# Optimization experiments

Measured on AMD Instinct MI355X. Metric: run time of the kernel, lower is better.

The kernel has to match this reference:

```python
import jax, jax.numpy as jnp
import numpy as np
from math import log

B, L, D = 2, 4096, 2048
H, Dh, C, KW = 16, 128, 64, 4
EPS = 1e-5
SCALE = 0.02


def setup_inputs() -> dict:
    key = jax.random.key(0)
    ks = jax.random.split(key, 16)
    rn = lambda k, shp, sc=SCALE: jax.random.normal(k, shp, jnp.float32) * sc
    # dt_bias built like the torch module
    dt = jnp.exp(jax.random.uniform(ks[7], (H,)) * (log(0.1) - log(0.001)) + log(0.001))
    dt = jnp.clip(dt, 0.0001, None)
    dt_bias = dt + jnp.log(-jnp.expm1(-dt))
    return {
        "x": jax.random.normal(ks[0], (B, L, D), jnp.float32),
        "Wq": rn(ks[1], (H * Dh, D)),
        "Wk": rn(ks[2], (H * Dh, D)),
        "Wv": rn(ks[3], (H * Dh, D)),
        "Wb": rn(ks[4], (H, D)),
        "Wa": rn(ks[5], (H, D)),
        "A_log": jnp.log(jax.random.uniform(ks[6], (H,), minval=0.01, maxval=16.0)),
        "dt_bias": dt_bias,
        "conv_q": rn(ks[8], (H * Dh, 1, KW), 0.2),
        "conv_k": rn(ks[9], (H * Dh, 1, KW), 0.2),
        "conv_v": rn(ks[10], (H * Dh, 1, KW), 0.2),
        "Wg": rn(ks[11], (H * Dh, D)),
        "norm_w": jnp.ones((Dh,), jnp.float32),
        "Wo": rn(ks[12], (D, H * Dh)),
        "S0": jnp.zeros((B, H, Dh, Dh), jnp.float32),
    }


def _causal_dwconv(x, w):
    # x: [B,L,Ch]; w: [Ch,1,KW] depthwise causal conv (left pad KW-1), then SiLU
    y = jax.lax.conv_general_dilated(
        x.transpose(0, 2, 1), w, (1,), [(KW - 1, 0)],
        feature_group_count=w.shape[0], dimension_numbers=("NCH", "OIH", "NCH"))
    return jax.nn.silu(y).transpose(0, 2, 1)


def reference(x, Wq, Wk, Wv, Wb, Wa, A_log, dt_bias, conv_q, conv_k, conv_v, Wg, norm_w, Wo, S0):
    q = _causal_dwconv(x @ Wq.T, conv_q).reshape(B, L, H, Dh).transpose(0, 2, 1, 3)  # [B,H,L,Dh]
    k = _causal_dwconv(x @ Wk.T, conv_k).reshape(B, L, H, Dh).transpose(0, 2, 1, 3)
    v = _causal_dwconv(x @ Wv.T, conv_v).reshape(B, L, H, Dh).transpose(0, 2, 1, 3)
    beta = jax.nn.sigmoid(x @ Wb.T).transpose(0, 2, 1)                                # [B,H,L]
    g = (-jnp.exp(A_log) * jax.nn.softplus(x @ Wa.T + dt_bias)).transpose(0, 2, 1)    # [B,H,L]
    l2 = lambda t: t / jnp.maximum(jnp.linalg.norm(t, axis=-1, keepdims=True), 1e-12)
    q = l2(q) / (Dh ** 0.5)
    k = l2(k)

    N = L // C  # chunks (L divisible by C)
    chop = lambda t: jnp.moveaxis(t.reshape(B, H, N, C, Dh), 2, 0)   # [N,B,H,C,Dh]
    qc, kc, vc = chop(q), chop(k), chop(v)
    betac = jnp.moveaxis(beta.reshape(B, H, N, C), 2, 0)[..., None]  # [N,B,H,C,1]
    gc = jnp.moveaxis(g.reshape(B, H, N, C), 2, 0)                   # [N,B,H,C]

    eye = jnp.eye(C, dtype=x.dtype)
    m_incl = jnp.tril(jnp.ones((C, C), bool))
    m_strict = jnp.tril(jnp.ones((C, C), bool), -1)

    def step(S, ch):
        Q, Kc, V, bet, gch = ch
        lg = jnp.cumsum(gch, axis=-1)          # log gamma, [B,H,C]
        gamma = jnp.exp(lg)
        lgC = lg[..., -1:]
        gCr = jnp.exp(lgC - lg)
        gammaC = jnp.exp(lgC)[..., None]       # [B,H,1,1]
        Qd = Q * gamma[..., None]
        Kd = gCr[..., None] * Kc
        Sd = S * gammaC
        Gam = lg[..., :, None] - lg[..., None, :]
        ratio = jnp.exp(jnp.where(m_strict, Gam, -jnp.inf))
        A = eye + bet * ratio * (Kc @ jnp.swapaxes(Kc, -1, -2))
        T = jax.scipy.linalg.solve_triangular(A, jnp.broadcast_to(eye, A.shape), lower=True)
        Wm = T @ (bet * gamma[..., None] * Kc)
        U = T @ (bet * V)
        St = jnp.swapaxes(S, -1, -2)
        GM = jnp.exp(jnp.where(m_incl, Gam, -jnp.inf))
        mid = U - Wm @ St                      # [B,H,C,Dh]
        O = Qd @ St + ((Q @ jnp.swapaxes(Kc, -1, -2)) * GM) @ mid
        S_new = Sd + jnp.swapaxes(mid, -1, -2) @ Kd
        return S_new, O

    S_fin, Os = jax.lax.scan(step, S0, (qc, kc, vc, betac, gc))
    o = Os.transpose(1, 0, 3, 2, 4).reshape(B, L, H, Dh)  # chunks -> [B,L,H,Dh]
    gate = (x @ Wg.T).reshape(B, L, H, Dh)
    # gated RMSNorm: rms-normalize o, scale by weight, gate with SiLU(g)
    o = o * jax.lax.rsqrt(jnp.mean(o * o, axis=-1, keepdims=True) + EPS) * norm_w * jax.nn.silu(gate)
    return (o.reshape(B, L, H * Dh) @ Wo.T, S_fin)
```

## Files before the change

kernel.cpp:

```cpp
#include <hip/hip_runtime.h>
#include <math.h>

#define B_   2
#define L_   4096
#define D_   2048
#define H_   16
#define DH   128
#define CH   64
#define NCH  64
#define HD   2048
#define BH   32
#define BHL  131072
#define PSZ  16777216ull

typedef unsigned short u16;
typedef __attribute__((ext_vector_type(8))) short bf16x8;
typedef __attribute__((ext_vector_type(4))) float f32x4;
#define MFMA16(a, b, c) __builtin_amdgcn_mfma_f32_16x16x32_bf16(a, b, c, 0, 0, 0)

static __device__ __forceinline__ float sigm(float x) { return 1.0f / (1.0f + expf(-x)); }

static __device__ __forceinline__ float b2f(u16 u) {
    union { float f; unsigned int i; } v; v.i = ((unsigned int)u) << 16; return v.f;
}
static __device__ __forceinline__ u16 f2b(float f) {
    union { float f; unsigned int i; } v; v.f = f;
    unsigned int r = v.i + 0x7fffu + ((v.i >> 16) & 1u);
    return (u16)(r >> 16);
}
static __device__ __forceinline__ void b8ld(const u16* p, float* d) {
    uint4 u = *(const uint4*)p;
    d[0] = b2f((u16)(u.x & 0xffff)); d[1] = b2f((u16)(u.x >> 16));
    d[2] = b2f((u16)(u.y & 0xffff)); d[3] = b2f((u16)(u.y >> 16));
    d[4] = b2f((u16)(u.z & 0xffff)); d[5] = b2f((u16)(u.z >> 16));
    d[6] = b2f((u16)(u.w & 0xffff)); d[7] = b2f((u16)(u.w >> 16));
}
static __device__ __forceinline__ void b8st(const float* s, u16* p) {
    uint4 u;
    u.x = (unsigned)f2b(s[0]) | ((unsigned)f2b(s[1]) << 16);
    u.y = (unsigned)f2b(s[2]) | ((unsigned)f2b(s[3]) << 16);
    u.z = (unsigned)f2b(s[4]) | ((unsigned)f2b(s[5]) << 16);
    u.w = (unsigned)f2b(s[6]) | ((unsigned)f2b(s[7]) << 16);
    *(uint4*)p = u;
}
static __device__ __forceinline__ void cstore(float* p, float v) { *p = v; }
static __device__ __forceinline__ void cstore(u16* p, float v) { *p = f2b(v); }

static __device__ __forceinline__ void async16(const u16* g, u16* l) {
    __builtin_amdgcn_global_load_lds(
        (const __attribute__((address_space(1))) unsigned int*)g,
        (__attribute__((address_space(3))) unsigned int*)l, 16, 0, 0);
}

static __device__ __forceinline__ void bar_lgkm() {
    asm volatile("s_waitcnt lgkmcnt(0)" ::: "memory");
    __builtin_amdgcn_sched_barrier(0);
    __builtin_amdgcn_s_barrier();
    __builtin_amdgcn_sched_barrier(0);
}
static __device__ __forceinline__ void wait_vm0() {
    asm volatile("s_waitcnt vmcnt(0)" ::: "memory");
    __builtin_amdgcn_sched_barrier(0);
}

__global__ __launch_bounds__(256) void cvt_f2b(const float* __restrict__ in,
                                               u16* __restrict__ out, int n8) {
    int i = blockIdx.x * 256 + threadIdx.x;
    if (i >= n8) return;
    float t[8];
    float4 a = *(const float4*)(in + (size_t)i * 8);
    float4 b = *(const float4*)(in + (size_t)i * 8 + 4);
    t[0] = a.x; t[1] = a.y; t[2] = a.z; t[3] = a.w;
    t[4] = b.x; t[5] = b.y; t[6] = b.z; t[7] = b.w;
    b8st(t, out + (size_t)i * 8);
}

template <typename TC>
__global__ __launch_bounds__(256) void gemm_bt_async(const u16* __restrict__ A,
                                                     const u16* __restrict__ Bm,
                                                     TC* __restrict__ Cm,
                                                     int M, int N, int K) {
    __shared__ __align__(16) u16 sA[128 * 64];
    __shared__ __align__(16) u16 sB[128 * 64];
    const int tid = threadIdx.x;
    const int w = tid >> 6, lane = tid & 63, lq = lane >> 4, ln = lane & 15;
    const int wm = w >> 1, wn = w & 1;
    const int nx = gridDim.x;
    const int lin = blockIdx.y * nx + blockIdx.x;
    const int chunk = (nx * gridDim.y) >> 3;
    const int wg = (lin & 7) * chunk + (lin >> 3);
    const int mbase = (wg / nx) * 128, nbase = (wg % nx) * 128;

    f32x4 acc[4][4];
#pragma unroll
    for (int mt = 0; mt < 4; mt++)
#pragma unroll
        for (int nt = 0; nt < 4; nt++) acc[mt][nt] = (f32x4){0.f, 0.f, 0.f, 0.f};

    for (int k0 = 0; k0 < K; k0 += 64) {
#pragma unroll
        for (int j = 0; j < 4; j++) {
            int c = tid + 256 * j;
            int row = c >> 3;
            int oct = (c & 7) ^ (row & 7);
            async16(A + (size_t)(mbase + row) * K + k0 + oct * 8, &sA[c * 8]);
            async16(Bm + (size_t)(nbase + row) * K + k0 + oct * 8, &sB[c * 8]);
        }
        __syncthreads();
#pragma unroll
        for (int ks = 0; ks < 2; ks++) {
            const int o = ks * 4 + lq;
            bf16x8 af[4], bfr[4];
#pragma unroll
            for (int mt = 0; mt < 4; mt++) {
                int m = wm * 64 + mt * 16 + ln;
                af[mt] = *(const bf16x8*)&sA[(m << 6) + ((o ^ (m & 7)) << 3)];
            }
#pragma unroll
            for (int nt = 0; nt < 4; nt++) {
                int nn = wn * 64 + nt * 16 + ln;
                bfr[nt] = *(const bf16x8*)&sB[(nn << 6) + ((o ^ (nn & 7)) << 3)];
            }
#pragma unroll
            for (int mt = 0; mt < 4; mt++)
#pragma unroll
                for (int nt = 0; nt < 4; nt++)
                    acc[mt][nt] = MFMA16(af[mt], bfr[nt], acc[mt][nt]);
        }
        __syncthreads();
    }
#pragma unroll
    for (int mt = 0; mt < 4; mt++)
#pragma unroll
        for (int nt = 0; nt < 4; nt++) {
            int col = nbase + wn * 64 + nt * 16 + ln;
#pragma unroll
            for (int r = 0; r < 4; r++) {
                int row = mbase + wm * 64 + mt * 16 + lq * 4 + r;
                cstore(Cm + (size_t)row * N + col, acc[mt][nt][r]);
            }
        }
}

__global__ __launch_bounds__(256) void conv_silu_norm(const u16* __restrict__ pre,
                                                      const float* __restrict__ w,
                                                      u16* __restrict__ out, int mode) {
    int wid = blockIdx.x * 4 + (threadIdx.x >> 6);
    int lane = threadIdx.x & 63;
    int l = wid & (L_ - 1);
    int bh = wid >> 12;
    int b = bh >> 4, h = bh & 15;

    float vals[2];
    float sumsq = 0.0f;
#pragma unroll
    for (int s = 0; s < 2; s++) {
        int d = lane + 64 * s;
        int c = h * DH + d;
        const u16* col = pre + (size_t)b * L_ * HD + c;
        float acc = 0.0f;
        if (l >= 3) {
            acc = w[c * 4 + 0] * b2f(col[(size_t)(l - 3) * HD]) +
                  w[c * 4 + 1] * b2f(col[(size_t)(l - 2) * HD]) +
                  w[c * 4 + 2] * b2f(col[(size_t)(l - 1) * HD]) +
                  w[c * 4 + 3] * b2f(col[(size_t)l * HD]);
        } else {
#pragma unroll
            for (int j = 0; j < 4; j++) {
                int ll = l - 3 + j;
                if (ll >= 0) acc += w[c * 4 + j] * b2f(col[(size_t)ll * HD]);
            }
        }
        float y = acc * sigm(acc);
        vals[s] = y;
        sumsq += y * y;
    }
    if (mode < 2) {
#pragma unroll
        for (int m = 32; m >= 1; m >>= 1) sumsq += __shfl_xor(sumsq, m, 64);
        float scale = 1.0f / fmaxf(sqrtf(sumsq), 1e-12f);
        if (mode == 0) scale *= 0.08838834764831843f;
        vals[0] *= scale;
        vals[1] *= scale;
    }
    u16* o = out + ((size_t)bh * L_ + l) * DH;
    o[lane] = f2b(vals[0]);
    o[lane + 64] = f2b(vals[1]);
}

__global__ __launch_bounds__(64) void proj_small(const float* __restrict__ x,
                                                 const float* __restrict__ Wb,
                                                 const float* __restrict__ Wa,
                                                 float* __restrict__ bpre,
                                                 float* __restrict__ apre) {
    int row = blockIdx.x;
    int lane = threadIdx.x;
    const float* xr = x + (size_t)row * D_;
    float xv[32];
#pragma unroll
    for (int j = 0; j < 32; j++) xv[j] = xr[lane + 64 * j];
    for (int h = 0; h < 16; h++) {
        const float* wr = Wb + (size_t)h * D_;
        float acc = 0.0f;
#pragma unroll
        for (int j = 0; j < 32; j++) acc += xv[j] * wr[lane + 64 * j];
#pragma unroll
        for (int m = 32; m >= 1; m >>= 1) acc += __shfl_xor(acc, m, 64);
        if (lane == 0) bpre[(size_t)row * 16 + h] = acc;
    }
    for (int h = 0; h < 16; h++) {
        const float* wr = Wa + (size_t)h * D_;
        float acc = 0.0f;
#pragma unroll
        for (int j = 0; j < 32; j++) acc += xv[j] * wr[lane + 64 * j];
#pragma unroll
        for (int m = 32; m >= 1; m >>= 1) acc += __shfl_xor(acc, m, 64);
        if (lane == 0) apre[(size_t)row * 16 + h] = acc;
    }
}

__global__ __launch_bounds__(256) void beta_g_k(const float* __restrict__ bpre,
                                                const float* __restrict__ apre,
                                                const float* __restrict__ A_log,
                                                const float* __restrict__ dt_bias,
                                                float* __restrict__ beta, float* __restrict__ g) {
    int gi = blockIdx.x * 256 + threadIdx.x;
    int l = gi & (L_ - 1);
    int bh = gi >> 12;
    int b = bh >> 4, h = bh & 15;
    float bp = bpre[((size_t)b * L_ + l) * 16 + h];
    float ap = apre[((size_t)b * L_ + l) * 16 + h] + dt_bias[h];
    float sp = (ap > 20.0f) ? ap : log1pf(expf(ap));
    beta[(size_t)bh * L_ + l] = 1.0f / (1.0f + expf(-bp));
    g[(size_t)bh * L_ + l] = -expf(A_log[h]) * sp;
}

__global__ __launch_bounds__(256) void prep_chunks(u16* __restrict__ q, u16* __restrict__ k,
                                                   u16* __restrict__ v,
                                                   const float* __restrict__ beta,
                                                   const float* __restrict__ g,
                                                   u16* __restrict__ Wm, u16* __restrict__ W2,
                                                   float* __restrict__ gamC) {
    __shared__ __align__(16) u16 sKb[64 * 136];
    __shared__ __align__(16) float sA[64 * 65];
    __shared__ __align__(16) float sT[64 * 68];
    __shared__ __align__(16) u16 sKsT[128 * 64];
    __shared__ float sLg[CH], sGam[CH], sGcr[CH], sBeta[CH];

    u16* sVsT = (u16*)sA;
    u16* sThi = (u16*)sT;
    u16* sTlo = (u16*)sT + 4096;

    const int cid = blockIdx.x;
    const int bh = cid >> 6, n = cid & 63;
    const int tid = threadIdx.x;
    const int w = tid >> 6, lane = tid & 63, lq = lane >> 4, ln = lane & 15;
    const size_t cbase = ((size_t)bh * L_ + (size_t)n * CH) * DH;
    u16* qw = q + cbase;
    u16* kw = k + cbase;
    u16* vc = v + cbase;

    bf16x8 aQ[4];
    {
        const u16* qrow = qw + (size_t)(w * 16 + ln) * DH;
#pragma unroll
        for (int ks = 0; ks < 4; ks++)
            aQ[ks] = *(const bf16x8*)(qrow + ks * 32 + lq * 8);
    }
#pragma unroll
    for (int rep = 0; rep < 4; rep++) {
        int f = tid + 256 * rep;
        int row = f >> 4, c8 = (f & 15) * 8;
        *(uint4*)&sKb[row * 136 + c8] = *(const uint4*)(kw + (size_t)row * DH + c8);
    }
    if (tid < 64) {
        float lg = g[(size_t)bh * L_ + (size_t)n * CH + tid];
#pragma unroll
        for (int off = 1; off < 64; off <<= 1) {
            float u = __shfl_up(lg, off, 64);
            if (tid >= off) lg += u;
        }
        float lgC = __shfl(lg, 63, 64);
        sLg[tid] = lg;
        sGam[tid] = expf(lg);
        sGcr[tid] = expf(lgC - lg);
        sBeta[tid] = beta[(size_t)bh * L_ + (size_t)n * CH + tid];
        if (tid == 63) gamC[cid] = expf(lgC);
    }
    __syncthreads();

    {
        f32x4 accA[4], accQ[4];
#pragma unroll
        for (int nt = 0; nt < 4; nt++) {
            accA[nt] = (f32x4){0.f, 0.f, 0.f, 0.f};
            accQ[nt] = (f32x4){0.f, 0.f, 0.f, 0.f};
        }
#pragma unroll
        for (int ks = 0; ks < 4; ks++) {
            int k0 = ks * 32 + lq * 8;
            bf16x8 aK = *(const bf16x8*)&sKb[(w * 16 + ln) * 136 + k0];
#pragma unroll
            for (int nt = 0; nt < 4; nt++) {
                bf16x8 bK = *(const bf16x8*)&sKb[(nt * 16 + ln) * 136 + k0];
                accA[nt] = MFMA16(aK, bK, accA[nt]);
                accQ[nt] = MFMA16(aQ[ks], bK, accQ[nt]);
            }
        }
        for (int idx = tid; idx < 64 * 68; idx += 256) sT[idx] = 0.f;
        u16* w2c = W2 + (size_t)cid * CH * CH;
#pragma unroll
        for (int nt = 0; nt < 4; nt++) {
            int j = nt * 16 + ln;
            float lgj = sLg[j];
#pragma unroll
            for (int r = 0; r < 4; r++) {
                int i = w * 16 + lq * 4 + r;
                float dexp = expf(fminf(sLg[i] - lgj, 0.f));
                sA[i * 65 + j] = (j < i) ? sBeta[i] * dexp * accA[nt][r] : 0.f;
                w2c[i * CH + j] = f2b((j <= i) ? accQ[nt][r] * dexp : 0.f);
            }
        }
    }
    __syncthreads();

    float colv[16];
    {
        const int i0 = w * 16;
        colv[0] = (ln == 0) ? 1.f : 0.f;
#pragma unroll
        for (int i = 1; i < 16; i++) {
            float acc = (ln == i) ? 1.f : 0.f;
#pragma unroll
            for (int kk = 0; kk < 15; kk++) {
                if (kk < i) acc -= sA[(i0 + i) * 65 + i0 + kk] * colv[kk];
            }
            colv[i] = acc;
        }
    }
#pragma unroll
    for (int rep = 0; rep < 4; rep++) {
        int f = tid + 256 * rep;
        int i = f >> 4, d8 = (f & 15) * 8;
        float tq[8];
        b8ld(qw + (size_t)i * DH + d8, tq);
        float sq = sGam[i];
#pragma unroll
        for (int jj = 0; jj < 8; jj++) tq[jj] *= sq;
        b8st(tq, qw + (size_t)i * DH + d8);
    }
    {
        int e = tid >> 1, qh = tid & 1;
#pragma unroll
        for (int oo = 0; oo < 4; oo++) {
            int i0 = qh * 32 + oo * 8;
            u16 op[8];
#pragma unroll
            for (int jj = 0; jj < 8; jj++)
                op[jj] = f2b(b2f(sKb[(i0 + jj) * 136 + e]) * sGcr[i0 + jj]);
            int slot = ((i0 >> 3) ^ (e & 7));
            uint4 pk;
            pk.x = (unsigned)op[0] | ((unsigned)op[1] << 16);
            pk.y = (unsigned)op[2] | ((unsigned)op[3] << 16);
            pk.z = (unsigned)op[4] | ((unsigned)op[5] << 16);
            pk.w = (unsigned)op[6] | ((unsigned)op[7] << 16);
            *(uint4*)(kw + e * 64 + slot * 8) = pk;
        }
    }
    if (lq == 0) {
#pragma unroll
        for (int i = 0; i < 16; i++) sT[(w * 16 + i) * 68 + w * 16 + ln] = colv[i];
    }
    __syncthreads();

    auto trijob = [&](int bi, int bj) {
        float accv[4] = {0.f, 0.f, 0.f, 0.f};
        for (int kb = bj; kb < bi; kb++) {
#pragma unroll
            for (int kk = 0; kk < 16; kk++) {
                float bv = sT[(kb * 16 + kk) * 68 + bj * 16 + ln];
#pragma unroll
                for (int r = 0; r < 4; r++)
                    accv[r] += sA[(bi * 16 + lq * 4 + r) * 65 + kb * 16 + kk] * bv;
            }
        }
        float xv[4] = {0.f, 0.f, 0.f, 0.f};
#pragma unroll
        for (int kk = 0; kk < 16; kk++) {
            float bv = __shfl(accv[kk & 3], (kk >> 2) * 16 + ln, 64);
#pragma unroll
            for (int r = 0; r < 4; r++)
                xv[r] -= sT[(bi * 16 + lq * 4 + r) * 68 + bi * 16 + kk] * bv;
        }
#pragma unroll
        for (int r = 0; r < 4; r++)
            sT[(bi * 16 + lq * 4 + r) * 68 + bj * 16 + ln] = xv[r];
    };
    if (w < 3) trijob(w + 1, w);
    __syncthreads();
    if (w < 2) trijob(w + 2, w);
    __syncthreads();
    if (w == 0) trijob(3, 0);
    __syncthreads();

    {
        int e = tid >> 1, qh = tid & 1;
#pragma unroll
        for (int oo = 0; oo < 4; oo++) {
            int i0 = qh * 32 + oo * 8;
            u16 op[8];
#pragma unroll
            for (int jj = 0; jj < 8; jj++) {
                int kkw = i0 + jj;
                op[jj] = f2b(b2f(sKb[kkw * 136 + e]) * (sBeta[kkw] * sGam[kkw]));
            }
            int slot = ((i0 >> 3) ^ (e & 7));
            uint4 pk;
            pk.x = (unsigned)op[0] | ((unsigned)op[1] << 16);
            pk.y = (unsigned)op[2] | ((unsigned)op[3] << 16);
            pk.z = (unsigned)op[4] | ((unsigned)op[5] << 16);
            pk.w = (unsigned)op[6] | ((unsigned)op[7] << 16);
            *(uint4*)&sKsT[e * 64 + slot * 8] = pk;
        }
    }
    float tvs[16];
    {
        int ti = tid >> 2, kks = (tid & 3) * 16;
#pragma unroll
        for (int j = 0; j < 16; j++) tvs[j] = sT[ti * 68 + kks + j];
    }
    __syncthreads();

    {
        int ti = tid >> 2, kks = (tid & 3) * 16;
#pragma unroll
        for (int h = 0; h < 2; h++) {
            u16 hi8[8], lo8[8];
#pragma unroll
            for (int j = 0; j < 8; j++) {
                float tv = tvs[h * 8 + j];
                u16 hb = f2b(tv);
                hi8[j] = hb;
                lo8[j] = f2b(tv - b2f(hb));
            }
            int io = (kks >> 3) + h;
            int slot = io ^ (ti & 7);
            uint4 ph, pl;
            ph.x = (unsigned)hi8[0] | ((unsigned)hi8[1] << 16);
            ph.y = (unsigned)hi8[2] | ((unsigned)hi8[3] << 16);
            ph.z = (unsigned)hi8[4] | ((unsigned)hi8[5] << 16);
            ph.w = (unsigned)hi8[6] | ((unsigned)hi8[7] << 16);
            pl.x = (unsigned)lo8[0] | ((unsigned)lo8[1] << 16);
            pl.y = (unsigned)lo8[2] | ((unsigned)lo8[3] << 16);
            pl.z = (unsigned)lo8[4] | ((unsigned)lo8[5] << 16);
            pl.w = (unsigned)lo8[6] | ((unsigned)lo8[7] << 16);
            *(uint4*)&sThi[ti * 64 + slot * 8] = ph;
            *(uint4*)&sTlo[ti * 64 + slot * 8] = pl;
        }
    }
#pragma unroll
    for (int rep = 0; rep < 4; rep++) {
        int f = tid + 256 * rep;
        int row = f >> 4, c8 = (f & 15) * 8;
        *(uint4*)&sKb[row * 136 + c8] = *(const uint4*)(vc + (size_t)row * DH + c8);
    }
    __syncthreads();

    {
        int e = tid >> 1, qh = tid & 1;
#pragma unroll
        for (int oo = 0; oo < 4; oo++) {
            int i0 = qh * 32 + oo * 8;
            u16 op[8];
#pragma unroll
            for (int jj = 0; jj < 8; jj++) {
                int kkw = i0 + jj;
                op[jj] = f2b(b2f(sKb[kkw * 136 + e]) * sBeta[kkw]);
            }
            int slot = ((i0 >> 3) ^ (e & 7));
            uint4 pk;
            pk.x = (unsigned)op[0] | ((unsigned)op[1] << 16);
            pk.y = (unsigned)op[2] | ((unsigned)op[3] << 16);
            pk.z = (unsigned)op[4] | ((unsigned)op[5] << 16);
            pk.w = (unsigned)op[6] | ((unsigned)op[7] << 16);
            *(uint4*)&sVsT[e * 64 + slot * 8] = pk;
        }
    }
    __syncthreads();

    {
        u16* wmc = Wm + (size_t)cid * CH * DH;
        bf16x8 bK[2][2], bV[2][2];
#pragma unroll
        for (int et = 0; et < 2; et++) {
            int eb = w * 32 + et * 16 + ln;
#pragma unroll
            for (int ks = 0; ks < 2; ks++) {
                int o = ks * 4 + lq;
                bK[et][ks] = *(const bf16x8*)&sKsT[eb * 64 + ((o ^ (eb & 7)) << 3)];
                bV[et][ks] = *(const bf16x8*)&sVsT[eb * 64 + ((o ^ (eb & 7)) << 3)];
            }
        }
#pragma unroll
        for (int it = 0; it < 4; it++) {
            int ia = it * 16 + ln;
            bf16x8 ahi[2], alo[2];
#pragma unroll
            for (int ks = 0; ks < 2; ks++) {
                int o = ks * 4 + lq;
                ahi[ks] = *(const bf16x8*)&sThi[ia * 64 + ((o ^ (ia & 7)) << 3)];
                alo[ks] = *(const bf16x8*)&sTlo[ia * 64 + ((o ^ (ia & 7)) << 3)];
            }
#pragma unroll
            for (int et = 0; et < 2; et++) {
                f32x4 aK = (f32x4){0.f, 0.f, 0.f, 0.f};
                f32x4 aV = (f32x4){0.f, 0.f, 0.f, 0.f};
#pragma unroll
                for (int ks = 0; ks < 2; ks++) {
                    aK = MFMA16(ahi[ks], bK[et][ks], aK);
                    aK = MFMA16(alo[ks], bK[et][ks], aK);
                    aV = MFMA16(ahi[ks], bV[et][ks], aV);
                    aV = MFMA16(alo[ks], bV[et][ks], aV);
                }
                int ecol = w * 32 + et * 16 + ln;
#pragma unroll
                for (int r = 0; r < 4; r++) {
                    int irow = it * 16 + lq * 4 + r;
                    wmc[(size_t)irow * DH + ecol] = f2b(aK[r]);
                    vc[(size_t)irow * DH + ecol] = f2b(aV[r]);
                }
            }
        }
    }
}

__global__ __launch_bounds__(256) void scan_mfma(const u16* __restrict__ Wm,
                                                 const u16* __restrict__ U,
                                                 const u16* __restrict__ Qd,
                                                 const u16* __restrict__ Kd,
                                                 const u16* __restrict__ W2,
                                                 const float* __restrict__ gamC,
                                                 const float* __restrict__ S0,
                                                 float* __restrict__ Og,
                                                 float* __restrict__ Sfin) {
    __shared__ __align__(16) u16 sWm[2][64 * 128];
    __shared__ __align__(16) u16 sQd[2][64 * 128];
    __shared__ __align__(16) u16 sW2[2][64 * 64];
    __shared__ __align__(16) u16 sKdT[2][128 * 64];
    __shared__ __align__(16) u16 sS[2][16 * 136];
    __shared__ __align__(16) u16 sMidT[16 * 72];

    const int bid = blockIdx.x;
    const int xcd = bid & 7, slot = bid >> 3;
    const int bh = xcd + 8 * (slot >> 3), dg = slot & 7, d0 = dg * 16;
    const int tid = threadIdx.x;
    const int w = tid >> 6, lane = tid & 63, lq = lane >> 4, ln = lane & 15;

    f32x4 S_t[2];
#pragma unroll
    for (int t2 = 0; t2 < 2; t2++)
#pragma unroll
        for (int r = 0; r < 4; r++)
            S_t[t2][r] = S0[(size_t)bh * DH * DH + (size_t)(d0 + lq * 4 + r) * DH + w * 32 + t2 * 16 + ln];

    auto stage_async = [&](int m, int p) {
        const size_t cid2 = (size_t)bh * NCH + m;
        const u16* wmc = Wm + cid2 * CH * DH;
        const size_t tb = ((size_t)bh * L_ + (size_t)m * CH) * DH;
        const u16* qc  = Qd + tb;
        const u16* kc  = Kd + tb;
        const u16* w2c = W2 + cid2 * CH * CH;
#pragma unroll
        for (int j = 0; j < 4; j++) {
            int c = tid + 256 * j;
            int row = c >> 4;
            int osrc = (c & 15) ^ (row & 7);
            async16(wmc + (size_t)row * DH + osrc * 8, &sWm[p][c * 8]);
            async16(qc  + (size_t)row * DH + osrc * 8, &sQd[p][c * 8]);
            async16(kc + (size_t)c * 8, &sKdT[p][c * 8]);
        }
#pragma unroll
        for (int j = 0; j < 2; j++) {
            int c = tid + 256 * j;
            int row = c >> 3;
            int osrc = (c & 7) ^ (row & 7);
            async16(w2c + (size_t)row * CH + osrc * 8, &sW2[p][c * 8]);
        }
    };
    auto write_ss = [&](int p) {
#pragma unroll
        for (int t2 = 0; t2 < 2; t2++)
#pragma unroll
            for (int r = 0; r < 4; r++)
                sS[p][(lq * 4 + r) * 136 + w * 32 + t2 * 16 + ln] = f2b(S_t[t2][r]);
    };

    u16 ureg[4], uregN[4];
    auto load_ureg = [&](int m, u16* dst) {
        const u16* uc = U + ((size_t)bh * L_ + (size_t)m * CH) * DH;
#pragma unroll
        for (int r = 0; r < 4; r++)
            dst[r] = uc[(size_t)(w * 16 + lq * 4 + r) * DH + d0 + ln];
    };

    stage_async(0, 0);
    load_ureg(0, ureg);
    float gCur = gamC[(size_t)bh * NCH];
    float gNext = 0.f;
    write_ss(0);
    wait_vm0();
    bar_lgkm();

    for (int n = 0; n < NCH; n++) {
        const int p = n & 1;
        const bool hasN = (n + 1 < NCH);
        if (hasN) {
            stage_async(n + 1, p ^ 1);
            load_ureg(n + 1, uregN);
            gNext = gamC[(size_t)bh * NCH + n + 1];
        }

        {
            f32x4 macc = (f32x4){0.f, 0.f, 0.f, 0.f};
            const int i = w * 16 + ln;
#pragma unroll
            for (int ks = 0; ks < 4; ks++) {
                int o = ks * 4 + lq;
                bf16x8 a = *(const bf16x8*)&sWm[p][i * 128 + ((o ^ (i & 7)) << 3)];
                bf16x8 b = *(const bf16x8*)&sS[p][ln * 136 + ks * 32 + lq * 8];
                macc = MFMA16(a, b, macc);
            }
#pragma unroll
            for (int r = 0; r < 4; r++) {
                int ii = w * 16 + lq * 4 + r;
                float mv = b2f(ureg[r]) - macc[r];
                sMidT[ln * 72 + ii] = f2b(mv);
            }
        }
        bar_lgkm();

        {
            f32x4 oacc = (f32x4){0.f, 0.f, 0.f, 0.f};
            const int i = w * 16 + ln;
#pragma unroll
            for (int ks = 0; ks < 4; ks++) {
                int o = ks * 4 + lq;
                bf16x8 a = *(const bf16x8*)&sQd[p][i * 128 + ((o ^ (i & 7)) << 3)];
                bf16x8 b = *(const bf16x8*)&sS[p][ln * 136 + ks * 32 + lq * 8];
                oacc = MFMA16(a, b, oacc);
            }
#pragma unroll
            for (int ks = 0; ks < 2; ks++) {
                int o = ks * 4 + lq;
                bf16x8 a = *(const bf16x8*)&sW2[p][i * 64 + ((o ^ (i & 7)) << 3)];
                bf16x8 b = *(const bf16x8*)&sMidT[ln * 72 + ks * 32 + lq * 8];
                oacc = MFMA16(a, b, oacc);
            }
#pragma unroll
            for (int r = 0; r < 4; r++) {
                int ii = w * 16 + lq * 4 + r;
                Og[((size_t)bh * L_ + (size_t)n * CH + ii) * DH + d0 + ln] = oacc[r];
            }
        }

#pragma unroll
        for (int t2 = 0; t2 < 2; t2++)
#pragma unroll
            for (int r = 0; r < 4; r++) S_t[t2][r] *= gCur;
#pragma unroll
        for (int ks = 0; ks < 2; ks++) {
            bf16x8 a = *(const bf16x8*)&sMidT[ln * 72 + ks * 32 + lq * 8];
#pragma unroll
            for (int t2 = 0; t2 < 2; t2++) {
                int e = (2 * w + t2) * 16 + ln;
                int o = ks * 4 + lq;
                bf16x8 b = *(const bf16x8*)&sKdT[p][e * 64 + ((o ^ (e & 7)) << 3)];
                S_t[t2] = MFMA16(a, b, S_t[t2]);
            }
        }

        if (hasN) {
            write_ss(p ^ 1);
#pragma unroll
            for (int r = 0; r < 4; r++) ureg[r] = uregN[r];
            gCur = gNext;
            wait_vm0();
            bar_lgkm();
        }
    }

#pragma unroll
    for (int t2 = 0; t2 < 2; t2++)
#pragma unroll
        for (int r = 0; r < 4; r++)
            Sfin[(size_t)bh * DH * DH + (size_t)(d0 + lq * 4 + r) * DH + w * 32 + t2 * 16 + ln] = S_t[t2][r];
}

__global__ __launch_bounds__(256) void epilogue_gate(const float* __restrict__ Ob,
                                                     const u16* __restrict__ gpre,
                                                     const float* __restrict__ norm_w,
                                                     u16* __restrict__ gated) {
    int wid = blockIdx.x * 4 + (threadIdx.x >> 6);
    int lane = threadIdx.x & 63;
    int l = wid & (L_ - 1);
    int bh = wid >> 12;
    int b = bh >> 4, h = bh & 15;
    const float* orow = Ob + ((size_t)bh * L_ + l) * DH;
    float o0 = orow[lane], o1 = orow[lane + 64];
    float ss = o0 * o0 + o1 * o1;
#pragma unroll
    for (int m = 32; m >= 1; m >>= 1) ss += __shfl_xor(ss, m, 64);
    float r = rsqrtf(ss * (1.0f / 128.0f) + 1e-5f);
    size_t gidx = ((size_t)b * L_ + l) * HD + h * DH;
    float gp0 = b2f(gpre[gidx + lane]), gp1 = b2f(gpre[gidx + lane + 64]);
    gated[gidx + lane] = f2b(o0 * r * norm_w[lane] * (gp0 * sigm(gp0)));
    gated[gidx + lane + 64] = f2b(o1 * r * norm_w[lane + 64] * (gp1 * sigm(gp1)));
}

extern "C" void kernel_launch(void* const* d_in, const int* in_sizes, int n_in,
                              void* d_out, int out_size, void* d_ws, size_t ws_size,
                              hipStream_t stream) {
    const float* x       = (const float*)d_in[0];
    const float* Wq      = (const float*)d_in[1];
    const float* Wk      = (const float*)d_in[2];
    const float* Wv      = (const float*)d_in[3];
    const float* Wb      = (const float*)d_in[4];
    const float* Wa      = (const float*)d_in[5];
    const float* A_log   = (const float*)d_in[6];
    const float* dt_bias = (const float*)d_in[7];
    const float* conv_q  = (const float*)d_in[8];
    const float* conv_k  = (const float*)d_in[9];
    const float* conv_v  = (const float*)d_in[10];
    const float* Wg      = (const float*)d_in[11];
    const float* norm_w  = (const float*)d_in[12];
    const float* Wo      = (const float*)d_in[13];
    const float* S0      = (const float*)d_in[14];
    float* out = (float*)d_out;

    u16* Pb = (u16*)d_ws;
    u16* Qb = Pb + PSZ;
    u16* Kb = Qb + PSZ;
    u16* Vb = Kb + PSZ;
    u16* W2b = Vb + PSZ;
    u16* xb  = W2b + PSZ / 2;
    u16* wbuf = xb + PSZ;
    float* bpre = (float*)(wbuf + 4194304);
    float* apre = bpre + BHL;
    float* betab = apre + BHL;
    float* gbuf = betab + BHL;
    float* gamC = gbuf + BHL;

    float* Obuf = out;
    float* Sfin = out + PSZ;

    dim3 gblk(16, 64);
    const int W8 = 2048 * 2048 / 8;

    cvt_f2b<<<8192, 256, 0, stream>>>(x, xb, (int)(PSZ / 8));
    cvt_f2b<<<2048, 256, 0, stream>>>(Wq, wbuf, W8);
    gemm_bt_async<u16><<<gblk, 256, 0, stream>>>(xb, wbuf, Pb, 8192, 2048, 2048);
    conv_silu_norm<<<32768, 256, 0, stream>>>(Pb, conv_q, Qb, 0);
    cvt_f2b<<<2048, 256, 0, stream>>>(Wk, wbuf, W8);
    gemm_bt_async<u16><<<gblk, 256, 0, stream>>>(xb, wbuf, Pb, 8192, 2048, 2048);
    conv_silu_norm<<<32768, 256, 0, stream>>>(Pb, conv_k, Kb, 1);
    cvt_f2b<<<2048, 256, 0, stream>>>(Wv, wbuf, W8);
    gemm_bt_async<u16><<<gblk, 256, 0, stream>>>(xb, wbuf, Pb, 8192, 2048, 2048);
    conv_silu_norm<<<32768, 256, 0, stream>>>(Pb, conv_v, Vb, 2);
    proj_small<<<8192, 64, 0, stream>>>(x, Wb, Wa, bpre, apre);
    beta_g_k<<<512, 256, 0, stream>>>(bpre, apre, A_log, dt_bias, betab, gbuf);
    prep_chunks<<<2048, 256, 0, stream>>>(Qb, Kb, Vb, betab, gbuf, Pb, W2b, gamC);
    scan_mfma<<<256, 256, 0, stream>>>(Pb, Vb, Qb, Kb, W2b, gamC, S0, Obuf, Sfin);
    cvt_f2b<<<2048, 256, 0, stream>>>(Wg, wbuf, W8);
    gemm_bt_async<u16><<<gblk, 256, 0, stream>>>(xb, wbuf, Vb, 8192, 2048, 2048);
    epilogue_gate<<<32768, 256, 0, stream>>>(Obuf, Vb, norm_w, Kb);
    cvt_f2b<<<2048, 256, 0, stream>>>(Wo, wbuf, W8);
    gemm_bt_async<float><<<gblk, 256, 0, stream>>>(Kb, wbuf, out, 8192, 2048, 2048);
}
```

Before: 1.030 ms.

## Use 256x256 double-buffered GEMM tiles with 512 threads

The bf16 GEMM grows from 128x128 tiles with 256 threads to 256x256 tiles with 512 threads (8 waves, 128x64 per wave). It double-buffers the LDS stages so the next K-tile's async loads overlap the current tile's MFMAs, and it raises wave priority during compute. The aim is more data reuse per byte loaded and hiding global load latency. In exchange LDS use reaches 128KB per block and the accumulators double, which lowers occupancy and yields only 256 blocks per GEMM.

```diff
diff --git a/kernel.cpp b/kernel.cpp
--- a/kernel.cpp
+++ b/kernel.cpp
@@ -76,67 +76,81 @@
 }
 
 template <typename TC>
-__global__ __launch_bounds__(256) void gemm_bt_async(const u16* __restrict__ A,
+__global__ __launch_bounds__(512) void gemm_bt_async(const u16* __restrict__ A,
                                                      const u16* __restrict__ Bm,
                                                      TC* __restrict__ Cm,
                                                      int M, int N, int K) {
-    __shared__ __align__(16) u16 sA[128 * 64];
-    __shared__ __align__(16) u16 sB[128 * 64];
+    __shared__ __align__(16) u16 sA[2][256 * 64];
+    __shared__ __align__(16) u16 sB[2][256 * 64];
     const int tid = threadIdx.x;
     const int w = tid >> 6, lane = tid & 63, lq = lane >> 4, ln = lane & 15;
-    const int wm = w >> 1, wn = w & 1;
+    const int wm = w >> 2, wn = w & 3;
     const int nx = gridDim.x;
     const int lin = blockIdx.y * nx + blockIdx.x;
     const int chunk = (nx * gridDim.y) >> 3;
     const int wg = (lin & 7) * chunk + (lin >> 3);
-    const int mbase = (wg / nx) * 128, nbase = (wg % nx) * 128;
-
-    f32x4 acc[4][4];
-#pragma unroll
-    for (int mt = 0; mt < 4; mt++)
+    const int mbase = (wg / nx) * 256, nbase = (wg % nx) * 256;
+
+    f32x4 acc[8][4];
+#pragma unroll
+    for (int mt = 0; mt < 8; mt++)
 #pragma unroll
         for (int nt = 0; nt < 4; nt++) acc[mt][nt] = (f32x4){0.f, 0.f, 0.f, 0.f};
 
-    for (int k0 = 0; k0 < K; k0 += 64) {
+    auto stage = [&](int kt, int p) {
+        const int k0 = kt * 64;
 #pragma unroll
         for (int j = 0; j < 4; j++) {
-            int c = tid + 256 * j;
+            int c = tid + 512 * j;
             int row = c >> 3;
             int oct = (c & 7) ^ (row & 7);
-            async16(A + (size_t)(mbase + row) * K + k0 + oct * 8, &sA[c * 8]);
-            async16(Bm + (size_t)(nbase + row) * K + k0 + oct * 8, &sB[c * 8]);
-        }
-        __syncthreads();
+            async16(A + (size_t)(mbase + row) * K + k0 + oct * 8, &sA[p][c * 8]);
+            async16(Bm + (size_t)(nbase + row) * K + k0 + oct * 8, &sB[p][c * 8]);
+        }
+    };
+
+    const int NT = K >> 6;
+    stage(0, 0);
+    wait_vm0();
+    __builtin_amdgcn_s_barrier();
+    __builtin_amdgcn_sched_barrier(0);
+
+    for (int t = 0; t < NT; t++) {
+        const int p = t & 1;
+        if (t + 1 < NT) stage(t + 1, p ^ 1);
+        __builtin_amdgcn_s_setprio(1);
 #pragma unroll
         for (int ks = 0; ks < 2; ks++) {
             const int o = ks * 4 + lq;
-            bf16x8 af[4], bfr[4];
-#pragma unroll
-            for (int mt = 0; mt < 4; mt++) {
-                int m = wm * 64 + mt * 16 + ln;
-                af[mt] = *(const bf16x8*)&sA[(m << 6) + ((o ^ (m & 7)) << 3)];
-            }
+            bf16x8 bfr[4];
 #pragma unroll
             for (int nt = 0; nt < 4; nt++) {
                 int nn = wn * 64 + nt * 16 + ln;
-                bfr[nt] = *(const bf16x8*)&sB[(nn << 6) + ((o ^ (nn & 7)) << 3)];
-            }
-#pragma unroll
-            for (int mt = 0; mt < 4; mt++)
+                bfr[nt] = *(const bf16x8*)&sB[p][(nn << 6) + ((o ^ (nn & 7)) << 3)];
+            }
+#pragma unroll
+            for (int mt = 0; mt < 8; mt++) {
+                int m = wm * 128 + mt * 16 + ln;
+                bf16x8 af = *(const bf16x8*)&sA[p][(m << 6) + ((o ^ (m & 7)) << 3)];
 #pragma unroll
                 for (int nt = 0; nt < 4; nt++)
-                    acc[mt][nt] = MFMA16(af[mt], bfr[nt], acc[mt][nt]);
-        }
-        __syncthreads();
-    }
-#pragma unroll
-    for (int mt = 0; mt < 4; mt++)
+                    acc[mt][nt] = MFMA16(af, bfr[nt], acc[mt][nt]);
+            }
+        }
+        __builtin_amdgcn_s_setprio(0);
+        if (t + 1 < NT) {
+            wait_vm0();
+            bar_lgkm();
+        }
+    }
+#pragma unroll
+    for (int mt = 0; mt < 8; mt++)
 #pragma unroll
         for (int nt = 0; nt < 4; nt++) {
             int col = nbase + wn * 64 + nt * 16 + ln;
 #pragma unroll
             for (int r = 0; r < 4; r++) {
-                int row = mbase + wm * 64 + mt * 16 + lq * 4 + r;
+                int row = mbase + wm * 128 + mt * 16 + lq * 4 + r;
                 cstore(Cm + (size_t)row * N + col, acc[mt][nt][r]);
             }
         }
@@ -753,26 +767,26 @@
     float* Obuf = out;
     float* Sfin = out + PSZ;
 
-    dim3 gblk(16, 64);
+    dim3 gblk(8, 32);
     const int W8 = 2048 * 2048 / 8;
 
     cvt_f2b<<<8192, 256, 0, stream>>>(x, xb, (int)(PSZ / 8));
     cvt_f2b<<<2048, 256, 0, stream>>>(Wq, wbuf, W8);
-    gemm_bt_async<u16><<<gblk, 256, 0, stream>>>(xb, wbuf, Pb, 8192, 2048, 2048);
+    gemm_bt_async<u16><<<gblk, 512, 0, stream>>>(xb, wbuf, Pb, 8192, 2048, 2048);
     conv_silu_norm<<<32768, 256, 0, stream>>>(Pb, conv_q, Qb, 0);
     cvt_f2b<<<2048, 256, 0, stream>>>(Wk, wbuf, W8);
-    gemm_bt_async<u16><<<gblk, 256, 0, stream>>>(xb, wbuf, Pb, 8192, 2048, 2048);
+    gemm_bt_async<u16><<<gblk, 512, 0, stream>>>(xb, wbuf, Pb, 8192, 2048, 2048);
     conv_silu_norm<<<32768, 256, 0, stream>>>(Pb, conv_k, Kb, 1);
     cvt_f2b<<<2048, 256, 0, stream>>>(Wv, wbuf, W8);
-    gemm_bt_async<u16><<<gblk, 256, 0, stream>>>(xb, wbuf, Pb, 8192, 2048, 2048);
+    gemm_bt_async<u16><<<gblk, 512, 0, stream>>>(xb, wbuf, Pb, 8192, 2048, 2048);
     conv_silu_norm<<<32768, 256, 0, stream>>>(Pb, conv_v, Vb, 2);
     proj_small<<<8192, 64, 0, stream>>>(x, Wb, Wa, bpre, apre);
     beta_g_k<<<512, 256, 0, stream>>>(bpre, apre, A_log, dt_bias, betab, gbuf);
     prep_chunks<<<2048, 256, 0, stream>>>(Qb, Kb, Vb, betab, gbuf, Pb, W2b, gamC);
     scan_mfma<<<256, 256, 0, stream>>>(Pb, Vb, Qb, Kb, W2b, gamC, S0, Obuf, Sfin);
     cvt_f2b<<<2048, 256, 0, stream>>>(Wg, wbuf, W8);
-    gemm_bt_async<u16><<<gblk, 256, 0, stream>>>(xb, wbuf, Vb, 8192, 2048, 2048);
+    gemm_bt_async<u16><<<gblk, 512, 0, stream>>>(xb, wbuf, Vb, 8192, 2048, 2048);
     epilogue_gate<<<32768, 256, 0, stream>>>(Obuf, Vb, norm_w, Kb);
     cvt_f2b<<<2048, 256, 0, stream>>>(Wo, wbuf, W8);
-    gemm_bt_async<float><<<gblk, 256, 0, stream>>>(Kb, wbuf, out, 8192, 2048, 2048);
-}
+    gemm_bt_async<float><<<gblk, 512, 0, stream>>>(Kb, wbuf, out, 8192, 2048, 2048);
+}
```

New measurement: 966.5 us. -6.2%, faster.
